# Kernel tuning notes

Measured on AMD Instinct MI355X. Metric: run time of the kernel, lower is better.

Reference implementation:

```python
import jax, jax.numpy as jnp
import numpy as np

N = 131072   # n_agents
K = 2        # k_neighbors = k_obstacles
H, C = 4, 128
HC = H * C   # 512
OBS_DIM = 37
OUT = 4


def setup_inputs() -> dict:
    key = jax.random.key(0)
    ks = jax.random.split(key, 40)
    s = 0.05
    def g(i, shape):
        return jax.random.normal(ks[i], shape, dtype=jnp.float32) * s
    inp = {"obs": jax.random.normal(ks[0], (N, OBS_DIM), dtype=jnp.float32)}
    # layer 0 (query_dim = 19)
    inp["wq0"] = g(1, (19, HC)); inp["wak0"] = g(2, (6, HC)); inp["wav0"] = g(3, (7, HC))
    inp["wok0"] = g(4, (2, HC)); inp["wov0"] = g(5, (2, HC))
    inp["apw0"] = g(6, (HC, C)); inp["apb0"] = jnp.zeros((C,), jnp.float32)
    inp["opw0"] = g(7, (HC, C)); inp["opb0"] = jnp.zeros((C,), jnp.float32)
    inp["fpw0"] = g(8, (2 * C, C)); inp["fpb0"] = jnp.zeros((C,), jnp.float32)
    inp["ca0"] = jnp.float32(1.0); inp["co0"] = jnp.float32(2.0)
    # layer 1 (query_dim = gnn_hidden_dim = 128)
    inp["wq1"] = g(9, (C, HC)); inp["wak1"] = g(10, (6, HC)); inp["wav1"] = g(11, (7, HC))
    inp["wok1"] = g(12, (2, HC)); inp["wov1"] = g(13, (2, HC))
    inp["apw1"] = g(14, (HC, C)); inp["apb1"] = jnp.zeros((C,), jnp.float32)
    inp["opw1"] = g(15, (HC, C)); inp["opb1"] = jnp.zeros((C,), jnp.float32)
    inp["fpw1"] = g(16, (2 * C, C)); inp["fpb1"] = jnp.zeros((C,), jnp.float32)
    inp["ca1"] = jnp.float32(1.0); inp["co1"] = jnp.float32(2.0)
    # output head
    inp["headw"] = g(17, (C, OUT)); inp["headb"] = jnp.zeros((OUT,), jnp.float32)
    return inp


def _forward(obs, wq0, wak0, wav0, wok0, wov0, apw0, apb0, opw0, opb0, fpw0, fpb0, ca0, co0,
             wq1, wak1, wav1, wok1, wov1, apw1, apb1, opw1, opb1, fpw1, fpb1, ca1, co1,
             headw, headb):
    n = obs.shape[0]
    scale = (C // H) ** -0.5  # matches torch: (out_channels // heads) ** -0.5

    # feature extraction per ObservationConfig (k=2)
    qf = jnp.concatenate([obs[:, 0:12], obs[:, 30:37]], axis=-1)        # [n, 19]
    nb = obs[:, 12:24].reshape(n, K, 6)                                  # neighbor keys [n,k,6]
    nbv = jnp.concatenate([nb, obs[:, 24:26][..., None]], axis=-1)       # + progress -> [n,k,7]
    ob = obs[:, 26:30].reshape(n, K, 2)                                  # obstacle k/v [n,k,2]
    apos = obs[:, 0:2]
    npos = nb[..., 0:2]
    opos = ob

    def attend(q, kfeat, vfeat, wk, wv, pw, pb, decay, pos_k):
        keys = (kfeat @ wk).reshape(n, K, H, C)
        vals = (vfeat @ wv).reshape(n, K, H, C)
        dist = jnp.linalg.norm(apos[:, None, :] - pos_k, axis=-1)        # [n,k]
        dw = jnp.exp(-decay * dist)                                      # [n,k]
        dot = jnp.einsum('nhc,nkhc->nhk', q, keys) * scale
        att = jax.nn.softmax(dot * dw[:, None, :], axis=-1)
        out = jnp.einsum('nhk,nkhc->nhc', att, vals).reshape(n, HC)
        return out @ pw + pb                                             # [n, C]

    def layer(qfeat, wq, wak, wav, wok, wov, apw, apb, opw, opb, fpw, fpb, ca, co):
        q = (qfeat @ wq).reshape(n, H, C)
        a = attend(q, nb, nbv, wak, wav, apw, apb, ca, npos)
        o = attend(q, ob, ob, wok, wov, opw, opb, co, opos)
        return jnp.concatenate([a, o], axis=-1) @ fpw + fpb              # [n, C]

    h = layer(qf, wq0, wak0, wav0, wok0, wov0, apw0, apb0, opw0, opb0, fpw0, fpb0, ca0, co0)
    h = layer(h, wq1, wak1, wav1, wok1, wov1, apw1, apb1, opw1, opb1, fpw1, fpb1, ca1, co1)
    return h @ headw + headb                                             # [n, OUT]


def reference(obs, wq0, wak0, wav0, wok0, wov0, apw0, apb0, opw0, opb0, fpw0, fpb0, ca0, co0,
              wq1, wak1, wav1, wok1, wov1, apw1, apb1, opw1, opb1, fpw1, fpb1, ca1, co1,
              headw, headb):
    return _forward(obs, wq0, wak0, wav0, wok0, wov0, apw0, apb0, opw0, opb0, fpw0, fpb0, ca0, co0,
                    wq1, wak1, wav1, wok1, wov1, apw1, apb1, opw1, opb1, fpw1, fpb1, ca1, co1,
                    headw, headb)
```

## Files before the change

### kernel.cpp

```cpp
#include <hip/hip_runtime.h>
#include <math.h>

#define NTH 256

typedef float v4f __attribute__((ext_vector_type(4)));

enum : int {
  WQ0_OFF = 0,
  M_OFF   = 608,
  TB_OFF  = 1760,
  AO1_OFF = 1792,
  B1H_OFF = 1936,
  TBL_N   = 1940,
  PREF_SCRATCH = 4096
};

__global__ __launch_bounds__(NTH) void prep_fused(
    const float* __restrict__ wq0,  const float* __restrict__ wak0, const float* __restrict__ wok0,
    const float* __restrict__ wav0, const float* __restrict__ wov0,
    const float* __restrict__ apw0, const float* __restrict__ opw0,
    const float* __restrict__ fpw0, const float* __restrict__ fpb0,
    const float* __restrict__ apb0, const float* __restrict__ opb0,
    const float* __restrict__ wq1,  const float* __restrict__ wak1, const float* __restrict__ wok1,
    const float* __restrict__ wav1, const float* __restrict__ wov1,
    const float* __restrict__ apw1, const float* __restrict__ opw1,
    const float* __restrict__ fpw1, const float* __restrict__ fpb1,
    const float* __restrict__ apb1, const float* __restrict__ opb1,
    const float* __restrict__ headw, const float* __restrict__ headb,
    const float* __restrict__ obs, float* __restrict__ ws, int n)
{
  const int b = blockIdx.x;
  const int tid = threadIdx.x;
  const float scale = 0.17677669529663687f;
  __shared__ float sm[768];

  if (b < 36) {
    const int t = b, h0 = t / 9, i0 = t % 9;
    float* sP = sm; float* sA = sm + 128; float* sG = sm + 256;
    if (tid < 128) {
      const float* w  = (i0 < 7 ? wav0 + i0 * 512 : wov0 + (i0 - 7) * 512) + h0 * 128;
      const float* pw = (i0 < 7 ? apw0 : opw0) + (h0 * 128) * 128 + tid;
      float acc = 0.f;
#pragma unroll 4
      for (int c = 0; c < 128; c++) acc += w[c] * pw[c * 128];
      sP[tid] = acc;
    }
    __syncthreads();
    if (tid < 128) {
      const float* f = fpw0 + (i0 < 7 ? 0 : 128 * 128) + tid;
      float acc = 0.f;
#pragma unroll 4
      for (int u = 0; u < 128; u++) acc += sP[u] * f[u * 128];
      sA[tid] = acc;
    }
    __syncthreads();
#pragma unroll
    for (int rep = 0; rep < 2; rep++) {
      const int hd = tid + rep * 256;
      float acc = 0.f;
#pragma unroll 4
      for (int c = 0; c < 128; c++) acc += sA[c] * wq1[c * 512 + hd];
      sG[hd] = acc;
    }
    __syncthreads();
    if (tid < 32) {
      const int h2 = tid >> 3, j2 = tid & 7;
      const float* wb = (j2 < 6 ? wak1 + j2 * 512 : wok1 + (j2 - 6) * 512) + h2 * 128;
      const float* g = sG + h2 * 128;
      float acc = 0.f;
#pragma unroll 4
      for (int d = 0; d < 128; d++) acc += g[d] * wb[d];
      ws[M_OFF + t * 32 + tid] = acc * scale;
    }
  } else if (b < 72) {
    const int t1 = b - 36, h = t1 / 9, i = t1 % 9;
    float* sP = sm; float* sR = sm + 128;
    if (tid < 128) {
      const float* w  = (i < 7 ? wav1 + i * 512 : wov1 + (i - 7) * 512) + h * 128;
      const float* pw = (i < 7 ? apw1 : opw1) + (h * 128) * 128 + tid;
      float acc = 0.f;
#pragma unroll 4
      for (int c = 0; c < 128; c++) acc += w[c] * pw[c * 128];
      sP[tid] = acc;
    }
    __syncthreads();
    if (tid < 128) {
      const float* f = fpw1 + (i < 7 ? 0 : 128 * 128) + tid;
      float acc = 0.f;
#pragma unroll 4
      for (int u = 0; u < 128; u++) acc += sP[u] * f[u * 128];
      sR[tid] = acc;
    }
    __syncthreads();
    if (tid < 4) {
      float acc = 0.f;
#pragma unroll 4
      for (int j = 0; j < 128; j++) acc += sR[j] * headw[j * 4 + tid];
      ws[AO1_OFF + t1 * 4 + tid] = acc;
    }
  } else if (b == 72) {
    float* sB = sm; float* sG = sm + 256;
    if (tid < 128) {
      float acc = fpb0[tid];
#pragma unroll 4
      for (int c = 0; c < 128; c++)
        acc += apb0[c] * fpw0[c * 128 + tid] + opb0[c] * fpw0[(128 + c) * 128 + tid];
      sB[tid] = acc;
    }
    __syncthreads();
#pragma unroll
    for (int rep = 0; rep < 2; rep++) {
      const int hd = tid + rep * 256;
      float acc = 0.f;
#pragma unroll 4
      for (int cc = 0; cc < 128; cc++) acc += sB[cc] * wq1[cc * 512 + hd];
      sG[hd] = acc;
    }
    __syncthreads();
    if (tid < 32) {
      const int h = tid >> 3, j = tid & 7;
      const float* wb = (j < 6 ? wak1 + j * 512 : wok1 + (j - 6) * 512) + h * 128;
      const float* g = sG + h * 128;
      float acc = 0.f;
#pragma unroll 4
      for (int d = 0; d < 128; d++) acc += g[d] * wb[d];
      ws[TB_OFF + tid] = acc * scale;
    }
  } else if (b == 73) {
    float* sB = sm;
    if (tid < 128) {
      float acc = fpb1[tid];
#pragma unroll 4
      for (int c = 0; c < 128; c++)
        acc += apb1[c] * fpw1[c * 128 + tid] + opb1[c] * fpw1[(128 + c) * 128 + tid];
      sB[tid] = acc;
    }
    __syncthreads();
    if (tid < 4) {
      float acc = headb[tid];
#pragma unroll 4
      for (int j = 0; j < 128; j++) acc += sB[j] * headw[j * 4 + tid];
      ws[B1H_OFF + tid] = acc;
    }
  } else if (b < 77) {
    const int idx = (b - 74) * NTH + tid;
    if (idx < 608) {
      const int j = idx & 7, r = (idx >> 3) % 19, h = idx / 152;
      const v4f* a4 = (const v4f*)(wq0 + r * 512 + h * 128);
      const v4f* b4 = (const v4f*)((j < 6 ? wak0 + j * 512 : wok0 + (j - 6) * 512) + h * 128);
      v4f va = (v4f)0.f;
#pragma unroll 8
      for (int c = 0; c < 32; c++) va += a4[c] * b4[c];
      ws[WQ0_OFF + idx] = (va[0] + va[1] + va[2] + va[3]) * scale;
    }
  } else {
    const int pid = (b - 77) * NTH + tid;
    const size_t total = (size_t)n * 37;
    float s = 0.f;
    for (size_t p = (size_t)pid * 32; p < total; p += (size_t)(512 - 77) * NTH * 32)
      s += obs[p];
    ws[PREF_SCRATCH + pid] = s;
  }
}

__global__ __launch_bounds__(NTH) void actor_main(
    const float* __restrict__ obs, const float* __restrict__ ws,
    const float* __restrict__ pca0, const float* __restrict__ pco0,
    const float* __restrict__ pca1, const float* __restrict__ pco1,
    float* __restrict__ out, int n)
{
  const int tid = threadIdx.x;
  const int gid = blockIdx.x * NTH + tid;

  __shared__ v4f sObsV[NTH * 37 / 4];
  float* sObs = (float*)sObsV;
  {
    const size_t total_f = (size_t)n * 37;
    const size_t v4base = (size_t)blockIdx.x * (NTH * 37 / 4);
    const v4f* src = (const v4f*)obs;
#pragma unroll
    for (int k = 0; k < 9; k++) {
      const size_t vi = v4base + k * NTH + tid;
      if (vi * 4 + 4 <= total_f) {
        sObsV[k * NTH + tid] = src[vi];
      } else {
#pragma unroll
        for (int e = 0; e < 4; e++) {
          const size_t f = vi * 4 + e;
          if (f < total_f) sObs[(k * NTH + tid) * 4 + e] = obs[f];
        }
      }
    }
    if (tid < 64) {
      const size_t vi = v4base + 9 * NTH + tid;
      if (vi * 4 + 4 <= total_f) {
        sObsV[9 * NTH + tid] = src[vi];
      } else {
#pragma unroll
        for (int e = 0; e < 4; e++) {
          const size_t f = vi * 4 + e;
          if (f < total_f) sObs[(9 * NTH + tid) * 4 + e] = obs[f];
        }
      }
    }
  }
  __syncthreads();
  if (gid >= n) return;

  const v4f* __restrict__ tbl = (const v4f*)ws;

  float o[37];
#pragma unroll
  for (int i = 0; i < 37; i++) o[i] = sObs[tid * 37 + i];

  float qf[19];
#pragma unroll
  for (int i = 0; i < 12; i++) qf[i] = o[i];
#pragma unroll
  for (int i = 0; i < 7; i++) qf[12 + i] = o[30 + i];
  float nb[2][6];
#pragma unroll
  for (int k2 = 0; k2 < 2; k2++)
#pragma unroll
    for (int i = 0; i < 6; i++) nb[k2][i] = o[12 + 6 * k2 + i];
  const float nbv6[2] = { o[24], o[25] };
  const float obf[2][2] = { { o[26], o[27] }, { o[28], o[29] } };
  const float ax = o[0], ay = o[1];

  float dista[2], disto[2];
#pragma unroll
  for (int k2 = 0; k2 < 2; k2++) {
    float dx = ax - nb[k2][0], dy = ay - nb[k2][1];
    dista[k2] = sqrtf(dx * dx + dy * dy);
    float ex = ax - obf[k2][0], ey = ay - obf[k2][1];
    disto[k2] = sqrtf(ex * ex + ey * ey);
  }
  const float ca0 = pca0[0], co0 = pco0[0], ca1 = pca1[0], co1 = pco1[0];
  float dwa0[2], dwo0[2], dwa1[2], dwo1[2];
#pragma unroll
  for (int k2 = 0; k2 < 2; k2++) {
    dwa0[k2] = __expf(-ca0 * dista[k2]);
    dwo0[k2] = __expf(-co0 * disto[k2]);
    dwa1[k2] = __expf(-ca1 * dista[k2]);
    dwo1[k2] = __expf(-co1 * disto[k2]);
  }

  v4f t0v[8];
#pragma unroll
  for (int z = 0; z < 8; z++) t0v[z] = (v4f)0.f;
#pragma unroll
  for (int h = 0; h < 4; h++) {
#pragma unroll
    for (int r = 0; r < 19; r++) {
      float q = qf[r];
      t0v[h * 2 + 0] += tbl[(h * 19 + r) * 2 + 0] * q;
      t0v[h * 2 + 1] += tbl[(h * 19 + r) * 2 + 1] * q;
    }
  }

  float wff[36];
#pragma unroll
  for (int h = 0; h < 4; h++) {
    float la[2], lo[2];
#pragma unroll
    for (int k2 = 0; k2 < 2; k2++) {
      float da = t0v[h*2][0]*nb[k2][0] + t0v[h*2][1]*nb[k2][1] + t0v[h*2][2]*nb[k2][2]
               + t0v[h*2][3]*nb[k2][3] + t0v[h*2+1][0]*nb[k2][4] + t0v[h*2+1][1]*nb[k2][5];
      la[k2] = da * dwa0[k2];
      float dof = t0v[h*2+1][2]*obf[k2][0] + t0v[h*2+1][3]*obf[k2][1];
      lo[k2] = dof * dwo0[k2];
    }
    float e  = __expf(la[1] - la[0]); float aa1 = e  / (1.f + e);  float aa0 = 1.f - aa1;
    float eo = __expf(lo[1] - lo[0]); float bo1 = eo / (1.f + eo); float bo0 = 1.f - bo1;
#pragma unroll
    for (int i = 0; i < 6; i++) wff[h * 9 + i] = aa0 * nb[0][i] + aa1 * nb[1][i];
    wff[h * 9 + 6] = aa0 * nbv6[0] + aa1 * nbv6[1];
    wff[h * 9 + 7] = bo0 * obf[0][0] + bo1 * obf[1][0];
    wff[h * 9 + 8] = bo0 * obf[0][1] + bo1 * obf[1][1];
  }

  v4f t1v[8];
#pragma unroll
  for (int q = 0; q < 8; q++) t1v[q] = tbl[440 + q];
#pragma unroll
  for (int t = 0; t < 36; t++) {
    float f = wff[t];
#pragma unroll
    for (int q = 0; q < 8; q++)
      t1v[q] += tbl[152 + t * 8 + q] * f;
  }

  float wf1f[36];
#pragma unroll
  for (int h = 0; h < 4; h++) {
    float la[2], lo[2];
#pragma unroll
    for (int k2 = 0; k2 < 2; k2++) {
      float da = t1v[h*2][0]*nb[k2][0] + t1v[h*2][1]*nb[k2][1] + t1v[h*2][2]*nb[k2][2]
               + t1v[h*2][3]*nb[k2][3] + t1v[h*2+1][0]*nb[k2][4] + t1v[h*2+1][1]*nb[k2][5];
      la[k2] = da * dwa1[k2];
      float dof = t1v[h*2+1][2]*obf[k2][0] + t1v[h*2+1][3]*obf[k2][1];
      lo[k2] = dof * dwo1[k2];
    }
    float e  = __expf(la[1] - la[0]); float aa1 = e  / (1.f + e);  float aa0 = 1.f - aa1;
    float eo = __expf(lo[1] - lo[0]); float bo1 = eo / (1.f + eo); float bo0 = 1.f - bo1;
#pragma unroll
    for (int i = 0; i < 6; i++) wf1f[h * 9 + i] = aa0 * nb[0][i] + aa1 * nb[1][i];
    wf1f[h * 9 + 6] = aa0 * nbv6[0] + aa1 * nbv6[1];
    wf1f[h * 9 + 7] = bo0 * obf[0][0] + bo1 * obf[1][0];
    wf1f[h * 9 + 8] = bo0 * obf[0][1] + bo1 * obf[1][1];
  }

  v4f acc = tbl[484];
#pragma unroll
  for (int t = 0; t < 36; t++)
    acc += tbl[448 + t] * wf1f[t];
  ((v4f*)out)[gid] = acc;
}

extern "C" void kernel_launch(void* const* d_in, const int* in_sizes, int n_in,
                              void* d_out, int out_size, void* d_ws, size_t ws_size,
                              hipStream_t stream)
{
  const float* obs  = (const float*)d_in[0];
  const float* wq0  = (const float*)d_in[1];
  const float* wak0 = (const float*)d_in[2];
  const float* wav0 = (const float*)d_in[3];
  const float* wok0 = (const float*)d_in[4];
  const float* wov0 = (const float*)d_in[5];
  const float* apw0 = (const float*)d_in[6];
  const float* apb0 = (const float*)d_in[7];
  const float* opw0 = (const float*)d_in[8];
  const float* opb0 = (const float*)d_in[9];
  const float* fpw0 = (const float*)d_in[10];
  const float* fpb0 = (const float*)d_in[11];
  const float* ca0  = (const float*)d_in[12];
  const float* co0  = (const float*)d_in[13];
  const float* wq1  = (const float*)d_in[14];
  const float* wak1 = (const float*)d_in[15];
  const float* wav1 = (const float*)d_in[16];
  const float* wok1 = (const float*)d_in[17];
  const float* wov1 = (const float*)d_in[18];
  const float* apw1 = (const float*)d_in[19];
  const float* apb1 = (const float*)d_in[20];
  const float* opw1 = (const float*)d_in[21];
  const float* opb1 = (const float*)d_in[22];
  const float* fpw1 = (const float*)d_in[23];
  const float* fpb1 = (const float*)d_in[24];
  const float* ca1  = (const float*)d_in[25];
  const float* co1  = (const float*)d_in[26];
  const float* headw = (const float*)d_in[27];
  const float* headb = (const float*)d_in[28];
  float* ws = (float*)d_ws;
  int n = in_sizes[0] / 37;

  prep_fused<<<512, NTH, 0, stream>>>(
      wq0, wak0, wok0, wav0, wov0, apw0, opw0, fpw0, fpb0, apb0, opb0,
      wq1, wak1, wok1, wav1, wov1, apw1, opw1, fpw1, fpb1, apb1, opb1,
      headw, headb, obs, ws, n);
  actor_main<<<(n + NTH - 1) / NTH, NTH, 0, stream>>>(
      obs, ws, ca0, co0, ca1, co1, (float*)d_out, n);
}
```

Before: 174.2 us.

## Split weight-folding prep into two parallel kernels and drop obs prefetch blocks

The single serial-chain prep kernel is replaced by two kernels. prepA computes the value-projection products, the wq1·wak1 transpose table, the biases and the transposed head weights, spread across many threads with vectorized loads. prepB then runs the short fpw and head reductions with an 8-way split reduction through shared memory. The blocks that read obs only to warm the cache for the main kernel are removed. This shortens each block's serial critical path at the cost of one extra kernel launch and the loss of the L2 warm-up for obs.

```diff
diff --git a/kernel.cpp b/kernel.cpp
--- a/kernel.cpp
+++ b/kernel.cpp
@@ -11,155 +11,172 @@
   TB_OFF  = 1760,
   AO1_OFF = 1792,
   B1H_OFF = 1936,
-  TBL_N   = 1940,
-  PREF_SCRATCH = 4096
+  PA0_OFF  = 2048,
+  PO0_OFF  = 5632,
+  PA1_OFF  = 6656,
+  PO1_OFF  = 10240,
+  WQ1T_OFF = 11264,
+  B0_OFF   = 15360,
+  BB1_OFF  = 15488,
+  HWT_OFF  = 15616,
+  WS_END   = 16128
 };
 
-__global__ __launch_bounds__(NTH) void prep_fused(
+__global__ __launch_bounds__(NTH) void prepA(
     const float* __restrict__ wq0,  const float* __restrict__ wak0, const float* __restrict__ wok0,
     const float* __restrict__ wav0, const float* __restrict__ wov0,
     const float* __restrict__ apw0, const float* __restrict__ opw0,
-    const float* __restrict__ fpw0, const float* __restrict__ fpb0,
-    const float* __restrict__ apb0, const float* __restrict__ opb0,
     const float* __restrict__ wq1,  const float* __restrict__ wak1, const float* __restrict__ wok1,
     const float* __restrict__ wav1, const float* __restrict__ wov1,
     const float* __restrict__ apw1, const float* __restrict__ opw1,
-    const float* __restrict__ fpw1, const float* __restrict__ fpb1,
-    const float* __restrict__ apb1, const float* __restrict__ opb1,
-    const float* __restrict__ headw, const float* __restrict__ headb,
-    const float* __restrict__ obs, float* __restrict__ ws, int n)
+    const float* __restrict__ fpw0, const float* __restrict__ fpw1,
+    const float* __restrict__ fpb0, const float* __restrict__ apb0, const float* __restrict__ opb0,
+    const float* __restrict__ fpb1, const float* __restrict__ apb1, const float* __restrict__ opb1,
+    const float* __restrict__ headw, float* __restrict__ ws)
 {
   const int b = blockIdx.x;
   const int tid = threadIdx.x;
   const float scale = 0.17677669529663687f;
-  __shared__ float sm[768];
-
-  if (b < 36) {
-    const int t = b, h0 = t / 9, i0 = t % 9;
-    float* sP = sm; float* sA = sm + 128; float* sG = sm + 256;
-    if (tid < 128) {
-      const float* w  = (i0 < 7 ? wav0 + i0 * 512 : wov0 + (i0 - 7) * 512) + h0 * 128;
-      const float* pw = (i0 < 7 ? apw0 : opw0) + (h0 * 128) * 128 + tid;
-      float acc = 0.f;
-#pragma unroll 4
-      for (int c = 0; c < 128; c++) acc += w[c] * pw[c * 128];
-      sP[tid] = acc;
-    }
-    __syncthreads();
-    if (tid < 128) {
-      const float* f = fpw0 + (i0 < 7 ? 0 : 128 * 128) + tid;
-      float acc = 0.f;
-#pragma unroll 4
-      for (int u = 0; u < 128; u++) acc += sP[u] * f[u * 128];
-      sA[tid] = acc;
-    }
-    __syncthreads();
-#pragma unroll
-    for (int rep = 0; rep < 2; rep++) {
-      const int hd = tid + rep * 256;
-      float acc = 0.f;
-#pragma unroll 4
-      for (int c = 0; c < 128; c++) acc += sA[c] * wq1[c * 512 + hd];
-      sG[hd] = acc;
-    }
-    __syncthreads();
-    if (tid < 32) {
-      const int h2 = tid >> 3, j2 = tid & 7;
-      const float* wb = (j2 < 6 ? wak1 + j2 * 512 : wok1 + (j2 - 6) * 512) + h2 * 128;
-      const float* g = sG + h2 * 128;
-      float acc = 0.f;
-#pragma unroll 4
-      for (int d = 0; d < 128; d++) acc += g[d] * wb[d];
-      ws[M_OFF + t * 32 + tid] = acc * scale;
-    }
-  } else if (b < 72) {
-    const int t1 = b - 36, h = t1 / 9, i = t1 % 9;
-    float* sP = sm; float* sR = sm + 128;
-    if (tid < 128) {
-      const float* w  = (i < 7 ? wav1 + i * 512 : wov1 + (i - 7) * 512) + h * 128;
-      const float* pw = (i < 7 ? apw1 : opw1) + (h * 128) * 128 + tid;
-      float acc = 0.f;
-#pragma unroll 4
-      for (int c = 0; c < 128; c++) acc += w[c] * pw[c * 128];
-      sP[tid] = acc;
-    }
-    __syncthreads();
-    if (tid < 128) {
-      const float* f = fpw1 + (i < 7 ? 0 : 128 * 128) + tid;
-      float acc = 0.f;
-#pragma unroll 4
-      for (int u = 0; u < 128; u++) acc += sP[u] * f[u * 128];
-      sR[tid] = acc;
-    }
-    __syncthreads();
-    if (tid < 4) {
-      float acc = 0.f;
-#pragma unroll 4
-      for (int j = 0; j < 128; j++) acc += sR[j] * headw[j * 4 + tid];
-      ws[AO1_OFF + t1 * 4 + tid] = acc;
-    }
-  } else if (b == 72) {
-    float* sB = sm; float* sG = sm + 256;
-    if (tid < 128) {
-      float acc = fpb0[tid];
-#pragma unroll 4
-      for (int c = 0; c < 128; c++)
-        acc += apb0[c] * fpw0[c * 128 + tid] + opb0[c] * fpw0[(128 + c) * 128 + tid];
-      sB[tid] = acc;
-    }
-    __syncthreads();
-#pragma unroll
-    for (int rep = 0; rep < 2; rep++) {
-      const int hd = tid + rep * 256;
-      float acc = 0.f;
-#pragma unroll 4
-      for (int cc = 0; cc < 128; cc++) acc += sB[cc] * wq1[cc * 512 + hd];
-      sG[hd] = acc;
-    }
-    __syncthreads();
-    if (tid < 32) {
-      const int h = tid >> 3, j = tid & 7;
-      const float* wb = (j < 6 ? wak1 + j * 512 : wok1 + (j - 6) * 512) + h * 128;
-      const float* g = sG + h * 128;
-      float acc = 0.f;
-#pragma unroll 4
-      for (int d = 0; d < 128; d++) acc += g[d] * wb[d];
-      ws[TB_OFF + tid] = acc * scale;
-    }
-  } else if (b == 73) {
-    float* sB = sm;
-    if (tid < 128) {
-      float acc = fpb1[tid];
-#pragma unroll 4
-      for (int c = 0; c < 128; c++)
-        acc += apb1[c] * fpw1[c * 128 + tid] + opb1[c] * fpw1[(128 + c) * 128 + tid];
-      sB[tid] = acc;
-    }
-    __syncthreads();
-    if (tid < 4) {
-      float acc = headb[tid];
-#pragma unroll 4
-      for (int j = 0; j < 128; j++) acc += sB[j] * headw[j * 4 + tid];
-      ws[B1H_OFF + tid] = acc;
-    }
-  } else if (b < 77) {
-    const int idx = (b - 74) * NTH + tid;
+
+  if (b < 9) {
+    const int idx = b * NTH + tid;
+    const float* w; const v4f* p4; int t4, outv;
+    if (idx < 896) {
+      int h = idx / 224, r = idx % 224, i = r >> 5; t4 = r & 31;
+      w = wav0 + i * 512 + h * 128; p4 = (const v4f*)(apw0 + h * 16384);
+      outv = (PA0_OFF >> 2) + (h * 7 + i) * 32 + t4;
+    } else if (idx < 1152) {
+      int k = idx - 896; int h = k >> 6, i = (k >> 5) & 1; t4 = k & 31;
+      w = wov0 + i * 512 + h * 128; p4 = (const v4f*)(opw0 + h * 16384);
+      outv = (PO0_OFF >> 2) + (h * 2 + i) * 32 + t4;
+    } else if (idx < 2048) {
+      int k = idx - 1152; int h = k / 224, r = k % 224, i = r >> 5; t4 = r & 31;
+      w = wav1 + i * 512 + h * 128; p4 = (const v4f*)(apw1 + h * 16384);
+      outv = (PA1_OFF >> 2) + (h * 7 + i) * 32 + t4;
+    } else {
+      int k = idx - 2048; int h = k >> 6, i = (k >> 5) & 1; t4 = k & 31;
+      w = wov1 + i * 512 + h * 128; p4 = (const v4f*)(opw1 + h * 16384);
+      outv = (PO1_OFF >> 2) + (h * 2 + i) * 32 + t4;
+    }
+    v4f acc = (v4f)0.f;
+#pragma unroll 32
+    for (int c = 0; c < 128; ++c) acc += w[c] * p4[c * 32 + t4];
+    ((v4f*)ws)[outv] = acc;
+  } else if (b < 25) {
+    const int idx = (b - 9) * NTH + tid;
+    const int cc = idx & 127, j = (idx >> 7) & 7, h = idx >> 10;
+    const v4f* a4 = (const v4f*)(wq1 + cc * 512 + h * 128);
+    const v4f* b4 = (const v4f*)(((j < 6) ? wak1 + j * 512 : wok1 + (j - 6) * 512) + h * 128);
+    v4f s = (v4f)0.f;
+#pragma unroll 16
+    for (int c4 = 0; c4 < 32; ++c4) s += a4[c4] * b4[c4];
+    ws[WQ1T_OFF + (h * 8 + j) * 128 + cc] = s[0] + s[1] + s[2] + s[3];
+  } else if (b < 28) {
+    const int idx = (b - 25) * NTH + tid;
     if (idx < 608) {
       const int j = idx & 7, r = (idx >> 3) % 19, h = idx / 152;
       const v4f* a4 = (const v4f*)(wq0 + r * 512 + h * 128);
-      const v4f* b4 = (const v4f*)((j < 6 ? wak0 + j * 512 : wok0 + (j - 6) * 512) + h * 128);
-      v4f va = (v4f)0.f;
-#pragma unroll 8
-      for (int c = 0; c < 32; c++) va += a4[c] * b4[c];
-      ws[WQ0_OFF + idx] = (va[0] + va[1] + va[2] + va[3]) * scale;
+      const v4f* b4 = (const v4f*)(((j < 6) ? wak0 + j * 512 : wok0 + (j - 6) * 512) + h * 128);
+      v4f s = (v4f)0.f;
+#pragma unroll 16
+      for (int c4 = 0; c4 < 32; ++c4) s += a4[c4] * b4[c4];
+      ws[WQ0_OFF + idx] = (s[0] + s[1] + s[2] + s[3]) * scale;
+    }
+  } else if (b == 28) {
+    __shared__ v4f red[256];
+    const int isB1 = tid >> 7;
+    const int s = tid & 127, j4 = s & 31, g = s >> 5;
+    const v4f* fp4 = (const v4f*)(isB1 ? fpw1 : fpw0);
+    const float* ab = isB1 ? apb1 : apb0;
+    const float* ob = isB1 ? opb1 : opb0;
+    const v4f* fb4 = (const v4f*)(isB1 ? fpb1 : fpb0);
+    v4f acc = (v4f)0.f;
+#pragma unroll 32
+    for (int c = g * 32; c < g * 32 + 32; ++c)
+      acc += ab[c] * fp4[c * 32 + j4] + ob[c] * fp4[(128 + c) * 32 + j4];
+    red[tid] = acc;
+    __syncthreads();
+    if (g == 0) {
+      v4f r = red[tid] + red[tid + 32] + red[tid + 64] + red[tid + 96] + fb4[j4];
+      ((v4f*)(ws + (isB1 ? BB1_OFF : B0_OFF)))[j4] = r;
     }
   } else {
-    const int pid = (b - 77) * NTH + tid;
-    const size_t total = (size_t)n * 37;
-    float s = 0.f;
-    for (size_t p = (size_t)pid * 32; p < total; p += (size_t)(512 - 77) * NTH * 32)
-      s += obs[p];
-    ws[PREF_SCRATCH + pid] = s;
+    for (int e = tid; e < 512; e += NTH) {
+      const int o = e >> 7, c = e & 127;
+      ws[HWT_OFF + e] = headw[c * 4 + o];
+    }
+  }
+}
+
+__global__ __launch_bounds__(NTH) void prepB(
+    const float* __restrict__ fpw0, const float* __restrict__ fpw1,
+    const float* __restrict__ headb, float* __restrict__ ws)
+{
+  const int b = blockIdx.x;
+  const int tid = threadIdx.x;
+  const float scale = 0.17677669529663687f;
+  __shared__ v4f sred[256];
+  __shared__ float sV[128];
+
+  if (b < 72) {
+    const int isL1 = (b >= 36) ? 1 : 0;
+    const int t = isL1 ? b - 36 : b;
+    const int h = t / 9, i = t % 9;
+    const int x4 = tid & 31, g = tid >> 5;
+    const float* P = ws + (i < 7
+        ? (isL1 ? PA1_OFF : PA0_OFF) + (h * 7 + i) * 128
+        : (isL1 ? PO1_OFF : PO0_OFF) + (h * 2 + (i - 7)) * 128);
+    const v4f* f4 = (const v4f*)((isL1 ? fpw1 : fpw0) + (i < 7 ? 0 : 16384));
+    v4f acc = (v4f)0.f;
+#pragma unroll
+    for (int u = g * 16; u < g * 16 + 16; ++u) acc += P[u] * f4[u * 32 + x4];
+    sred[tid] = acc;
+    __syncthreads();
+    if (g == 0) {
+      v4f r = sred[x4];
+#pragma unroll
+      for (int q = 1; q < 8; ++q) r += sred[q * 32 + x4];
+      ((v4f*)sV)[x4] = r;
+    }
+    __syncthreads();
+    if (!isL1) {
+      if (tid < 32) {
+        const int h2 = tid >> 3, j2 = tid & 7;
+        const v4f* W4 = (const v4f*)(ws + WQ1T_OFF + (h2 * 8 + j2) * 128);
+        const v4f* A4 = (const v4f*)sV;
+        v4f a = (v4f)0.f;
+#pragma unroll
+        for (int c4 = 0; c4 < 32; ++c4) a += A4[c4] * W4[c4];
+        ws[M_OFF + t * 32 + tid] = (a[0] + a[1] + a[2] + a[3]) * scale;
+      }
+    } else {
+      if (tid < 4) {
+        const v4f* H4 = (const v4f*)(ws + HWT_OFF + tid * 128);
+        const v4f* R4 = (const v4f*)sV;
+        v4f a = (v4f)0.f;
+#pragma unroll
+        for (int c4 = 0; c4 < 32; ++c4) a += R4[c4] * H4[c4];
+        ws[AO1_OFF + t * 4 + tid] = a[0] + a[1] + a[2] + a[3];
+      }
+    }
+  } else {
+    if (tid < 32) {
+      const int h = tid >> 3, j = tid & 7;
+      const v4f* B4 = (const v4f*)(ws + B0_OFF);
+      const v4f* W4 = (const v4f*)(ws + WQ1T_OFF + (h * 8 + j) * 128);
+      v4f a = (v4f)0.f;
+#pragma unroll
+      for (int c4 = 0; c4 < 32; ++c4) a += B4[c4] * W4[c4];
+      ws[TB_OFF + tid] = (a[0] + a[1] + a[2] + a[3]) * scale;
+    } else if (tid < 36) {
+      const int o = tid - 32;
+      const v4f* B4 = (const v4f*)(ws + BB1_OFF);
+      const v4f* H4 = (const v4f*)(ws + HWT_OFF + o * 128);
+      v4f a = (v4f)0.f;
+#pragma unroll
+      for (int c4 = 0; c4 < 32; ++c4) a += B4[c4] * H4[c4];
+      ws[B1H_OFF + o] = a[0] + a[1] + a[2] + a[3] + headb[o];
+    }
   }
 }
 
@@ -354,10 +371,11 @@
   float* ws = (float*)d_ws;
   int n = in_sizes[0] / 37;
 
-  prep_fused<<<512, NTH, 0, stream>>>(
-      wq0, wak0, wok0, wav0, wov0, apw0, opw0, fpw0, fpb0, apb0, opb0,
-      wq1, wak1, wok1, wav1, wov1, apw1, opw1, fpw1, fpb1, apb1, opb1,
-      headw, headb, obs, ws, n);
+  prepA<<<30, NTH, 0, stream>>>(
+      wq0, wak0, wok0, wav0, wov0, apw0, opw0,
+      wq1, wak1, wok1, wav1, wov1, apw1, opw1,
+      fpw0, fpw1, fpb0, apb0, opb0, fpb1, apb1, opb1, headw, ws);
+  prepB<<<73, NTH, 0, stream>>>(fpw0, fpw1, headb, ws);
   actor_main<<<(n + NTH - 1) / NTH, NTH, 0, stream>>>(
       obs, ws, ca0, co0, ca1, co1, (float*)d_out, n);
 }
```

Measured after the change: 150.6 us. 1.16x faster.
